# Kernel tuning notes

Measured on AMD Instinct MI355X. Metric: run time of the kernel, lower is better.

The kernel has to match this reference:

```python
import jax, jax.numpy as jnp
import numpy as np

B, S = 64, 256
VOCAB, DL, DA, DV = 30522, 300, 74, 35
DH, GH, LH, RH = 128, 64, 128, 128  # modality dim, proj-GRU hidden, LSTM hidden, RGN hidden


def _gru_dir(x, Wi, Wh, bi, bh):
    # x: [B,S,D] -> [B,S,H]; torch GRU gate order (r, z, n)
    xg = x @ Wi + bi  # [B,S,3H] precomputed input projections
    H = Wh.shape[0]
    def step(h, xg_t):
        hg = h @ Wh + bh
        xr, xz, xn = jnp.split(xg_t, 3, axis=-1)
        hr, hz, hn = jnp.split(hg, 3, axis=-1)
        r = jax.nn.sigmoid(xr + hr)
        z = jax.nn.sigmoid(xz + hz)
        n = jnp.tanh(xn + r * hn)
        h = (1.0 - z) * n + z * h
        return h, h
    h0 = jnp.zeros((x.shape[0], H), x.dtype)
    _, ys = jax.lax.scan(step, h0, jnp.swapaxes(xg, 0, 1))
    return jnp.swapaxes(ys, 0, 1)


def _bigru(x, Wi, Wh, bi, bh):
    f = _gru_dir(x, Wi[0], Wh[0], bi[0], bh[0])
    b = _gru_dir(x[:, ::-1], Wi[1], Wh[1], bi[1], bh[1])[:, ::-1]
    return jnp.concatenate([f, b], axis=-1)


def _lstm_dir(x, Wi, Wh, bi, bh):
    xg = x @ Wi + bi  # [B,S,4H]; torch LSTM gate order (i, f, g, o)
    H = Wh.shape[0]
    def step(carry, xg_t):
        h, c = carry
        g = xg_t + h @ Wh + bh
        i, f, gg, o = jnp.split(g, 4, axis=-1)
        c = jax.nn.sigmoid(f) * c + jax.nn.sigmoid(i) * jnp.tanh(gg)
        h = jax.nn.sigmoid(o) * jnp.tanh(c)
        return (h, c), h
    z = jnp.zeros((x.shape[0], H), x.dtype)
    _, ys = jax.lax.scan(step, (z, z), jnp.swapaxes(xg, 0, 1))
    return jnp.swapaxes(ys, 0, 1)


def _bilstm(x, Wi, Wh, bi, bh):
    f = _lstm_dir(x, Wi[0], Wh[0], bi[0], bh[0])
    b = _lstm_dir(x[:, ::-1], Wi[1], Wh[1], bi[1], bh[1])[:, ::-1]
    return jnp.concatenate([f, b], axis=-1)


def _rgn_scan(x, h0, Wx, Wh, b):
    # RGNCell: gated recurrent cell (GRU-style), returns final state [B,H]
    xg = x @ Wx + b  # [B,S,3H]
    def step(h, xg_t):
        hg = h @ Wh
        xr, xz, xn = jnp.split(xg_t, 3, axis=-1)
        hr, hz, hn = jnp.split(hg, 3, axis=-1)
        r = jax.nn.sigmoid(xr + hr)
        z = jax.nn.sigmoid(xz + hz)
        n = jnp.tanh(xn + r * hn)
        return (1.0 - z) * n + z * h, None
    h, _ = jax.lax.scan(step, h0, jnp.swapaxes(xg, 0, 1))
    return h


def _xattn(q, kv):
    # parameter-free scaled dot-product cross-modal attention (JCAF)
    scale = 1.0 / np.sqrt(q.shape[-1]).astype(np.float32)
    s = jnp.einsum('bsd,btd->bst', q, kv) * scale
    return jnp.einsum('bst,btd->bsd', jax.nn.softmax(s, axis=-1), kv)


def _forward(sentences, acoustic, video, state0, state1, emb,
             proj_l_W, proj_l_b, proj_a_W, proj_a_b, proj_v_W, proj_v_b,
             gru_Wi, gru_Wh, gru_bi, gru_bh,
             lstm_Wi, lstm_Wh, lstm_bi, lstm_bh,
             rgn_Wx, rgn_Wh, rgn_b, fc1_W, fc1_b, fc2_W, fc2_b):
    enc = emb[sentences]                          # LanguageEmbeddingLayer: [B,S,DL]
    # SeqEncoder: project each modality to 128-d (dropout off in eval)
    seq_l = enc @ proj_l_W + proj_l_b             # [B,S,128]
    seq_a = acoustic @ proj_a_W + proj_a_b
    seq_v = video @ proj_v_W + proj_v_b
    # project_l/a/v: bidirectional GRU 128 -> 2*64 = 128
    x_l = _bigru(seq_l, gru_Wi[0], gru_Wh[0], gru_bi[0], gru_bh[0])
    x_a = _bigru(seq_a, gru_Wi[1], gru_Wh[1], gru_bi[1], gru_bh[1])
    x_v = _bigru(seq_v, gru_Wi[2], gru_Wh[2], gru_bi[2], gru_bh[2])
    # JCAF: each modality enriched by cross-attention to the other two
    fin_txt = x_l + _xattn(x_l, x_a) + _xattn(x_l, x_v)
    fin_aud = x_a + _xattn(x_a, x_l) + _xattn(x_a, x_v)
    fin_vis = x_v + _xattn(x_v, x_l) + _xattn(x_v, x_a)
    tstep = jnp.concatenate([fin_txt, fin_aud, fin_vis], axis=-1)      # [B,S,384]
    step_fusion = _bilstm(tstep, lstm_Wi, lstm_Wh, lstm_bi, lstm_bh)   # [B,S,256]
    # two custom RGNCell recurrences: forward sweep + reversed sweep
    out0 = _rgn_scan(step_fusion, state0, rgn_Wx[0], rgn_Wh[0], rgn_b[0])
    out1 = _rgn_scan(step_fusion[:, ::-1], state1, rgn_Wx[1], rgn_Wh[1], rgn_b[1])
    h = jax.nn.leaky_relu((out0 + out1) @ fc1_W + fc1_b)
    return h @ fc2_W + fc2_b                     # [B,1]


def setup_inputs():
    keys = iter(jax.random.split(jax.random.key(0), 48))
    def rn(shape, s=0.05):
        return jax.random.normal(next(keys), shape, jnp.float32) * s
    return {
        'sentences': jax.random.randint(next(keys), (B, S), 0, VOCAB),
        'acoustic': jax.random.normal(next(keys), (B, S, DA), jnp.float32),
        'video': jax.random.normal(next(keys), (B, S, DV), jnp.float32),
        'state0': jax.random.normal(next(keys), (B, RH), jnp.float32),
        'state1': jax.random.normal(next(keys), (B, RH), jnp.float32),
        'emb': rn((VOCAB, DL), 0.1),
        'proj_l_W': rn((DL, DH)), 'proj_l_b': rn((DH,)),
        'proj_a_W': rn((DA, DH)), 'proj_a_b': rn((DH,)),
        'proj_v_W': rn((DV, DH)), 'proj_v_b': rn((DH,)),
        'gru_Wi': rn((3, 2, DH, 3 * GH)), 'gru_Wh': rn((3, 2, GH, 3 * GH)),
        'gru_bi': rn((3, 2, 3 * GH)), 'gru_bh': rn((3, 2, 3 * GH)),
        'lstm_Wi': rn((2, 3 * DH, 4 * LH)), 'lstm_Wh': rn((2, LH, 4 * LH)),
        'lstm_bi': rn((2, 4 * LH)), 'lstm_bh': rn((2, 4 * LH)),
        'rgn_Wx': rn((2, 2 * LH, 3 * RH)), 'rgn_Wh': rn((2, RH, 3 * RH)),
        'rgn_b': rn((2, 3 * RH)),
        'fc1_W': rn((RH, 32)), 'fc1_b': rn((32,)),
        'fc2_W': rn((32, 1)), 'fc2_b': rn((1,)),
    }


def reference(sentences, acoustic, video, state0, state1, emb,
              proj_l_W, proj_l_b, proj_a_W, proj_a_b, proj_v_W, proj_v_b,
              gru_Wi, gru_Wh, gru_bi, gru_bh,
              lstm_Wi, lstm_Wh, lstm_bi, lstm_bh,
              rgn_Wx, rgn_Wh, rgn_b, fc1_W, fc1_b, fc2_W, fc2_b):
    return _forward(sentences, acoustic, video, state0, state1, emb,
                    proj_l_W, proj_l_b, proj_a_W, proj_a_b, proj_v_W, proj_v_b,
                    gru_Wi, gru_Wh, gru_bi, gru_bh,
                    lstm_Wi, lstm_Wh, lstm_bi, lstm_bh,
                    rgn_Wx, rgn_Wh, rgn_b, fc1_W, fc1_b, fc2_W, fc2_b)
```

## Files before the change

kernel.cpp:

```cpp
#include <hip/hip_runtime.h>

#define WS_SEQ      0LL
#define WS_XGGRU    6291456LL
#define WS_X        0LL
#define WS_TSTEP    18874368LL
#define WS_S        6291456LL
#define WS_XGLSTM   0LL
#define WS_SF       16777216LL
#define WS_XGRGN    0LL
#define WS_OUT0     20971520LL

__device__ __forceinline__ float sigf(float x) { return 1.f / (1.f + __expf(-x)); }
__device__ __forceinline__ float rl(float v, int i) {
    return __int_as_float(__builtin_amdgcn_readlane(__float_as_int(v), i));
}

typedef float vf16 __attribute__((ext_vector_type(16)));

#define LD16(V, P, S) { _Pragma("unroll") \
    for (int _j = 0; _j < 16; ++_j) (V)[_j] = (P)[_j * (S)]; }
#define DOT16(ACC, V, H, B) { _Pragma("unroll") \
    for (int _j = 0; _j < 16; ++_j) (ACC) = fmaf(rl((H), (B) + _j), (V)[_j], (ACC)); }

__device__ __forceinline__ void gemm_body(
    const float* __restrict__ Ab, int lda, const int* __restrict__ idx,
    const float* __restrict__ Wb, int wld, int wtrans,
    const float* __restrict__ bb,
    float* __restrict__ Cb, int ldc,
    int K, float alpha, int accum)
{
    int m0 = blockIdx.y * 64, n0 = blockIdx.x * 64;
    int t = threadIdx.x;
    int tx = t & 7, ty = t >> 3;

    __shared__ __align__(16) float As[16][68];
    __shared__ __align__(16) float Ws[16][68];

    float acc[8][8];
#pragma unroll
    for (int i = 0; i < 8; ++i)
#pragma unroll
        for (int j = 0; j < 8; ++j) acc[i][j] = 0.f;

    long long arow[4];
#pragma unroll
    for (int i = 0; i < 4; ++i) {
        int m = (t + i * 64) >> 2;
        arow[i] = idx ? (long long)idx[m0 + m] : (long long)(m0 + m);
    }
    const bool a_vec = ((lda & 3) == 0);

    for (int k0 = 0; k0 < K; k0 += 16) {
#pragma unroll
        for (int i = 0; i < 4; ++i) {
            int j = t + i * 64;
            int m = j >> 2, kq = j & 3;
            int kk = k0 + kq * 4;
            const float* p = Ab + arow[i] * (long long)lda + kk;
            float4 v = {0.f, 0.f, 0.f, 0.f};
            if (a_vec && kk + 3 < K) {
                v = *(const float4*)p;
            } else {
                if (kk + 0 < K) v.x = p[0];
                if (kk + 1 < K) v.y = p[1];
                if (kk + 2 < K) v.z = p[2];
                if (kk + 3 < K) v.w = p[3];
            }
            As[kq * 4 + 0][m] = v.x; As[kq * 4 + 1][m] = v.y;
            As[kq * 4 + 2][m] = v.z; As[kq * 4 + 3][m] = v.w;
        }
        if (!wtrans) {
#pragma unroll
            for (int i = 0; i < 4; ++i) {
                int j = t + i * 64;
                int k = j >> 4, nq = j & 15;
                float4 v = {0.f, 0.f, 0.f, 0.f};
                if (k0 + k < K)
                    v = *(const float4*)(Wb + (long long)(k0 + k) * wld + n0 + nq * 4);
                *(float4*)&Ws[k][nq * 4] = v;
            }
        } else {
#pragma unroll
            for (int i = 0; i < 4; ++i) {
                int j = t + i * 64;
                int n = j >> 2, kq = j & 3;
                int kk = k0 + kq * 4;
                const float* p = Wb + (long long)(n0 + n) * wld + kk;
                float4 v = {0.f, 0.f, 0.f, 0.f};
                if (kk + 3 < K) v = *(const float4*)p;
                else {
                    if (kk + 0 < K) v.x = p[0];
                    if (kk + 1 < K) v.y = p[1];
                    if (kk + 2 < K) v.z = p[2];
                    if (kk + 3 < K) v.w = p[3];
                }
                Ws[kq * 4 + 0][n] = v.x; Ws[kq * 4 + 1][n] = v.y;
                Ws[kq * 4 + 2][n] = v.z; Ws[kq * 4 + 3][n] = v.w;
            }
        }
        __syncthreads();
#pragma unroll
        for (int k = 0; k < 16; ++k) {
            float4 a0 = *(const float4*)&As[k][ty * 8];
            float4 a1 = *(const float4*)&As[k][ty * 8 + 4];
            float4 b0 = *(const float4*)&Ws[k][tx * 8];
            float4 b1 = *(const float4*)&Ws[k][tx * 8 + 4];
            float av[8] = {a0.x, a0.y, a0.z, a0.w, a1.x, a1.y, a1.z, a1.w};
            float bv[8] = {b0.x, b0.y, b0.z, b0.w, b1.x, b1.y, b1.z, b1.w};
#pragma unroll
            for (int i = 0; i < 8; ++i)
#pragma unroll
                for (int j = 0; j < 8; ++j)
                    acc[i][j] = fmaf(av[i], bv[j], acc[i][j]);
        }
        __syncthreads();
    }

#pragma unroll
    for (int i = 0; i < 8; ++i) {
        long long gm = m0 + ty * 8 + i;
#pragma unroll
        for (int jq = 0; jq < 2; ++jq) {
            float* cp = Cb + gm * ldc + n0 + tx * 8 + jq * 4;
            float4 v;
            v.x = alpha * acc[i][jq * 4 + 0]; v.y = alpha * acc[i][jq * 4 + 1];
            v.z = alpha * acc[i][jq * 4 + 2]; v.w = alpha * acc[i][jq * 4 + 3];
            if (bb) {
                const float* bp = bb + n0 + tx * 8 + jq * 4;
                v.x += bp[0]; v.y += bp[1]; v.z += bp[2]; v.w += bp[3];
            }
            if (accum) {
                float4 o = *(const float4*)cp;
                v.x += o.x; v.y += o.y; v.z += o.z; v.w += o.w;
            }
            *(float4*)cp = v;
        }
    }
}

__global__ __launch_bounds__(64) void gemm_k(
    const float* __restrict__ A, long long a_z, int a_zdiv, int lda,
    const int* __restrict__ idx,
    const float* __restrict__ W, long long w_z, int wld, int wtrans,
    const float* __restrict__ bias, int bias_z,
    float* __restrict__ C, long long c_z, int ldc,
    int K, float alpha, int accum)
{
    int z = blockIdx.z;
    gemm_body(A + (long long)(z / a_zdiv) * a_z, lda, idx,
              W + (long long)z * w_z, wld, wtrans,
              bias ? bias + (long long)z * bias_z : nullptr,
              C + (long long)z * c_z, ldc, K, alpha, accum);
}

__global__ __launch_bounds__(64) void att_score_k(
    const float* __restrict__ X, float* __restrict__ S,
    int q0, int q1, int q2, int k0, int k1, int k2)
{
    int z = blockIdx.z;
    int pair = z >> 6, b = z & 63;
    int qi = pair == 0 ? q0 : (pair == 1 ? q1 : q2);
    int ki = pair == 0 ? k0 : (pair == 1 ? k1 : k2);
    gemm_body(X + (long long)qi * 2097152 + (long long)b * 32768, 128, nullptr,
              X + (long long)ki * 2097152 + (long long)b * 32768, 128, 1,
              nullptr,
              S + (long long)z * 65536, 256, 128, 0.08838834764831845f, 0);
}

__global__ __launch_bounds__(64) void att_apply_k(
    const float* __restrict__ S, const float* __restrict__ X,
    float* __restrict__ tstep,
    int q0, int q1, int q2, int k0, int k1, int k2)
{
    int z = blockIdx.z;
    int pair = z >> 6, b = z & 63;
    int qi = pair == 0 ? q0 : (pair == 1 ? q1 : q2);
    int ki = pair == 0 ? k0 : (pair == 1 ? k1 : k2);
    gemm_body(S + (long long)z * 65536, 256, nullptr,
              X + (long long)ki * 2097152 + (long long)b * 32768, 128, 0,
              nullptr,
              tstep + (long long)qi * 128 + (long long)b * 98304, 384,
              256, 1.f, 1);
}

__global__ __launch_bounds__(256) void copy_tstep_k(const float* __restrict__ x,
                                                    float* __restrict__ tstep)
{
    int o = blockIdx.x * 256 + threadIdx.x;
    int c = o % 384;
    int row = o / 384;
    int m = c >> 7, cc = c & 127;
    tstep[o] = x[(long long)m * 2097152 + (long long)row * 128 + cc];
}

__global__ __launch_bounds__(256) void softmax_k(float* __restrict__ S)
{
    int wave = threadIdx.x >> 6, lane = threadIdx.x & 63;
    int row = blockIdx.x * 4 + wave;
    float* p = S + (long long)row * 256;
    float v[4];
    float mx = -1e30f;
#pragma unroll
    for (int i = 0; i < 4; ++i) { v[i] = p[lane + i * 64]; mx = fmaxf(mx, v[i]); }
#pragma unroll
    for (int off = 32; off > 0; off >>= 1) mx = fmaxf(mx, __shfl_xor(mx, off));
    float sum = 0.f;
#pragma unroll
    for (int i = 0; i < 4; ++i) { v[i] = __expf(v[i] - mx); sum += v[i]; }
#pragma unroll
    for (int off = 32; off > 0; off >>= 1) sum += __shfl_xor(sum, off);
    float inv = 1.f / sum;
#pragma unroll
    for (int i = 0; i < 4; ++i) p[lane + i * 64] = v[i] * inv;
}

__global__ __launch_bounds__(192) void gru_rec_k(const float* __restrict__ xg,
                                                 const float* __restrict__ Wh,
                                                 const float* __restrict__ bh,
                                                 float* __restrict__ xout)
{
    int b = blockIdx.x, z = blockIdx.y;
    int m = z >> 1, d = z & 1;
    int tid = threadIdx.x, lane = tid & 63;
    int c = tid;
    const float* Whz = Wh + (long long)z * 12288;
    const float* wp = Whz + c;
    vf16 W0, W1, W2, W3;
    LD16(W0, wp + 0 * 16 * 192, 192); LD16(W1, wp + 1 * 16 * 192, 192);
    LD16(W2, wp + 2 * 16 * 192, 192); LD16(W3, wp + 3 * 16 * 192, 192);
    float bias = bh[z * 192 + c];

    __shared__ float hs[64];
    __shared__ float g[192];
    int n = tid;
    float h = 0.f;
    const float* xgb = xg + (long long)z * 3145728 + (long long)b * 49152;
    float* xob = xout + (long long)m * 2097152 + (long long)b * 32768 + d * 64;
    float x_r = 0, x_z = 0, x_n = 0;
    if (tid < 64) {
        hs[n] = 0.f;
        int tt0 = d ? 255 : 0;
        const float* xr = xgb + tt0 * 192;
        x_r = xr[n]; x_z = xr[64 + n]; x_n = xr[128 + n];
    }
    __syncthreads();

#pragma unroll 1
    for (int t = 0; t < 256; ++t) {
        int tt = d ? 255 - t : t;
        float nx_r = 0, nx_z = 0, nx_n = 0;
        if (tid < 64 && t < 255) {
            const float* xr = xgb + (d ? tt - 1 : tt + 1) * 192;
            nx_r = xr[n]; nx_z = xr[64 + n]; nx_n = xr[128 + n];
        }
        float hv = hs[lane];
        float s0 = bias, s1 = 0.f, s2 = 0.f, s3 = 0.f;
        DOT16(s0, W0, hv, 0);  DOT16(s1, W1, hv, 16);
        DOT16(s2, W2, hv, 32); DOT16(s3, W3, hv, 48);
        g[c] = (s0 + s1) + (s2 + s3);
        __syncthreads();
        if (tid < 64) {
            float r  = sigf(x_r + g[n]);
            float zz = sigf(x_z + g[64 + n]);
            float nn = tanhf(x_n + r * g[128 + n]);
            h = (1.f - zz) * nn + zz * h;
            hs[n] = h;
            xob[tt * 128 + n] = h;
            x_r = nx_r; x_z = nx_z; x_n = nx_n;
        }
        __syncthreads();
    }
}

__global__ __launch_bounds__(1024) void lstm_rec_k(const float* __restrict__ xg,
                                                   const float* __restrict__ Wh,
                                                   const float* __restrict__ bh,
                                                   float* __restrict__ sf)
{
    int b = blockIdx.x, d = blockIdx.y;
    int tid = threadIdx.x, lane = tid & 63;
    int kh = tid >> 9;
    int c  = tid & 511;
    const float* Whz = Wh + (long long)d * 65536;
    const float* wp = Whz + (long long)(kh * 64) * 512 + c;
    vf16 W0, W1, W2, W3;
    LD16(W0, wp + 0 * 16 * 512, 512); LD16(W1, wp + 1 * 16 * 512, 512);
    LD16(W2, wp + 2 * 16 * 512, 512); LD16(W3, wp + 3 * 16 * 512, 512);

    __shared__ float hs[128];
    __shared__ float part[1024];
    int n = tid;
    float b_i = 0, b_f = 0, b_g = 0, b_o = 0, h = 0.f, cst = 0.f;
    const float* xgb = xg + (long long)d * 8388608 + (long long)b * 131072;
    float* sfb = sf + (long long)b * 65536 + d * 128;
    float x_i = 0, x_f = 0, x_g = 0, x_o = 0;
    if (tid < 128) {
        b_i = bh[d * 512 + n];       b_f = bh[d * 512 + 128 + n];
        b_g = bh[d * 512 + 256 + n]; b_o = bh[d * 512 + 384 + n];
        hs[n] = 0.f;
        int tt0 = d ? 255 : 0;
        const float* xr = xgb + tt0 * 512;
        x_i = xr[n]; x_f = xr[128 + n]; x_g = xr[256 + n]; x_o = xr[384 + n];
    }
    __syncthreads();

#pragma unroll 1
    for (int t = 0; t < 256; ++t) {
        int tt = d ? 255 - t : t;
        float nx_i = 0, nx_f = 0, nx_g = 0, nx_o = 0;
        if (tid < 128 && t < 255) {
            const float* xr = xgb + (d ? tt - 1 : tt + 1) * 512;
            nx_i = xr[n]; nx_f = xr[128 + n]; nx_g = xr[256 + n]; nx_o = xr[384 + n];
        }
        float hv = hs[kh * 64 + lane];
        float s0 = 0.f, s1 = 0.f, s2 = 0.f, s3 = 0.f;
        DOT16(s0, W0, hv, 0);  DOT16(s1, W1, hv, 16);
        DOT16(s2, W2, hv, 32); DOT16(s3, W3, hv, 48);
        part[kh * 512 + c] = (s0 + s1) + (s2 + s3);
        __syncthreads();
        if (tid < 128) {
            float iv = part[n]       + part[512 + n]       + b_i + x_i;
            float fv = part[128 + n] + part[512 + 128 + n] + b_f + x_f;
            float gv = part[256 + n] + part[512 + 256 + n] + b_g + x_g;
            float ov = part[384 + n] + part[512 + 384 + n] + b_o + x_o;
            cst = sigf(fv) * cst + sigf(iv) * tanhf(gv);
            h = sigf(ov) * tanhf(cst);
            hs[n] = h;
            sfb[tt * 256 + n] = h;
            x_i = nx_i; x_f = nx_f; x_g = nx_g; x_o = nx_o;
        }
        __syncthreads();
    }
}

__global__ __launch_bounds__(768) void rgn_rec_k(const float* __restrict__ xg,
                                                 const float* __restrict__ Wh,
                                                 const float* __restrict__ state0,
                                                 const float* __restrict__ state1,
                                                 float* __restrict__ outbase)
{
    int b = blockIdx.x, d = blockIdx.y;
    int tid = threadIdx.x, lane = tid & 63;
    int kh = (tid >= 384) ? 1 : 0;
    int c  = tid - kh * 384;
    const float* Whz = Wh + (long long)d * 49152;
    const float* wp = Whz + (long long)(kh * 64) * 384 + c;
    vf16 W0, W1, W2, W3;
    LD16(W0, wp + 0 * 16 * 384, 384); LD16(W1, wp + 1 * 16 * 384, 384);
    LD16(W2, wp + 2 * 16 * 384, 384); LD16(W3, wp + 3 * 16 * 384, 384);

    __shared__ float hs[128];
    __shared__ float part[768];
    int n = tid;
    float h = 0.f;
    const float* st = d ? state1 : state0;
    const float* xgb = xg + (long long)d * 6291456 + (long long)b * 98304;
    float x_r = 0, x_z = 0, x_n = 0;
    if (tid < 128) {
        h = st[b * 128 + n];
        hs[n] = h;
        int tt0 = d ? 255 : 0;
        const float* xr = xgb + tt0 * 384;
        x_r = xr[n]; x_z = xr[128 + n]; x_n = xr[256 + n];
    }
    __syncthreads();

#pragma unroll 1
    for (int t = 0; t < 256; ++t) {
        int tt = d ? 255 - t : t;
        float nx_r = 0, nx_z = 0, nx_n = 0;
        if (tid < 128 && t < 255) {
            const float* xr = xgb + (d ? tt - 1 : tt + 1) * 384;
            nx_r = xr[n]; nx_z = xr[128 + n]; nx_n = xr[256 + n];
        }
        float hv = hs[kh * 64 + lane];
        float s0 = 0.f, s1 = 0.f, s2 = 0.f, s3 = 0.f;
        DOT16(s0, W0, hv, 0);  DOT16(s1, W1, hv, 16);
        DOT16(s2, W2, hv, 32); DOT16(s3, W3, hv, 48);
        part[kh * 384 + c] = (s0 + s1) + (s2 + s3);
        __syncthreads();
        if (tid < 128) {
            float pr = part[n]       + part[384 + n];
            float pz = part[128 + n] + part[384 + 128 + n];
            float pn = part[256 + n] + part[384 + 256 + n];
            float r  = sigf(x_r + pr);
            float zz = sigf(x_z + pz);
            float nn = tanhf(x_n + r * pn);
            h = (1.f - zz) * nn + zz * h;
            hs[n] = h;
            x_r = nx_r; x_z = nx_z; x_n = nx_n;
        }
        __syncthreads();
    }
    if (tid < 128) outbase[(long long)d * 8192 + b * 128 + n] = h;
}

__global__ __launch_bounds__(256) void fc_k(const float* __restrict__ o01,
                                            const float* __restrict__ f1W,
                                            const float* __restrict__ f1b,
                                            const float* __restrict__ f2W,
                                            const float* __restrict__ f2b,
                                            float* __restrict__ out)
{
    __shared__ float s[8192];
    __shared__ float h1[2048];
    int tid = threadIdx.x;
    for (int e = tid; e < 8192; e += 256) s[e] = o01[e] + o01[8192 + e];
    __syncthreads();
    for (int o = tid; o < 2048; o += 256) {
        int b = o >> 5, q = o & 31;
        float acc = f1b[q];
        for (int k = 0; k < 128; ++k) acc += s[b * 128 + k] * f1W[k * 32 + q];
        h1[o] = acc >= 0.f ? acc : 0.01f * acc;
    }
    __syncthreads();
    if (tid < 64) {
        float acc = f2b[0];
        for (int q = 0; q < 32; ++q) acc += h1[tid * 32 + q] * f2W[q];
        out[tid] = acc;
    }
}

extern "C" void kernel_launch(void* const* d_in, const int* in_sizes, int n_in,
                              void* d_out, int out_size, void* d_ws, size_t ws_size,
                              hipStream_t stream)
{
    const int*   sent     = (const int*)  d_in[0];
    const float* acoustic = (const float*)d_in[1];
    const float* video    = (const float*)d_in[2];
    const float* state0   = (const float*)d_in[3];
    const float* state1   = (const float*)d_in[4];
    const float* emb      = (const float*)d_in[5];
    const float* plW = (const float*)d_in[6],  *plb = (const float*)d_in[7];
    const float* paW = (const float*)d_in[8],  *pab = (const float*)d_in[9];
    const float* pvW = (const float*)d_in[10], *pvb = (const float*)d_in[11];
    const float* gWi = (const float*)d_in[12], *gWh = (const float*)d_in[13];
    const float* gbi = (const float*)d_in[14], *gbh = (const float*)d_in[15];
    const float* lWi = (const float*)d_in[16], *lWh = (const float*)d_in[17];
    const float* lbi = (const float*)d_in[18], *lbh = (const float*)d_in[19];
    const float* rWx = (const float*)d_in[20], *rWh = (const float*)d_in[21];
    const float* rb  = (const float*)d_in[22];
    const float* f1W = (const float*)d_in[23], *f1b = (const float*)d_in[24];
    const float* f2W = (const float*)d_in[25], *f2b = (const float*)d_in[26];
    float* ws  = (float*)d_ws;
    float* out = (float*)d_out;

    dim3 blk(64);

    gemm_k<<<dim3(2, 256, 1), blk, 0, stream>>>(emb, 0, 1, 300, sent,
        plW, 0, 128, 0, plb, 0, ws + WS_SEQ, 0, 128, 300, 1.f, 0);
    gemm_k<<<dim3(2, 256, 1), blk, 0, stream>>>(acoustic, 0, 1, 74, nullptr,
        paW, 0, 128, 0, pab, 0, ws + WS_SEQ + 2097152, 0, 128, 74, 1.f, 0);
    gemm_k<<<dim3(2, 256, 1), blk, 0, stream>>>(video, 0, 1, 35, nullptr,
        pvW, 0, 128, 0, pvb, 0, ws + WS_SEQ + 4194304, 0, 128, 35, 1.f, 0);

    gemm_k<<<dim3(3, 256, 6), blk, 0, stream>>>(ws + WS_SEQ, 2097152, 2, 128, nullptr,
        gWi, 24576, 192, 0, gbi, 192, ws + WS_XGGRU, 3145728, 192, 128, 1.f, 0);

    gru_rec_k<<<dim3(64, 6), dim3(192), 0, stream>>>(ws + WS_XGGRU, gWh, gbh, ws + WS_X);

    copy_tstep_k<<<dim3(24576), dim3(256), 0, stream>>>(ws + WS_X, ws + WS_TSTEP);

    att_score_k<<<dim3(4, 4, 192), blk, 0, stream>>>(ws + WS_X, ws + WS_S,
        0, 1, 2, 1, 0, 0);
    softmax_k<<<dim3(12288), dim3(256), 0, stream>>>(ws + WS_S);
    att_apply_k<<<dim3(2, 4, 192), blk, 0, stream>>>(ws + WS_S, ws + WS_X,
        ws + WS_TSTEP, 0, 1, 2, 1, 0, 0);
    att_score_k<<<dim3(4, 4, 192), blk, 0, stream>>>(ws + WS_X, ws + WS_S,
        0, 1, 2, 2, 2, 1);
    softmax_k<<<dim3(12288), dim3(256), 0, stream>>>(ws + WS_S);
    att_apply_k<<<dim3(2, 4, 192), blk, 0, stream>>>(ws + WS_S, ws + WS_X,
        ws + WS_TSTEP, 0, 1, 2, 2, 2, 1);

    gemm_k<<<dim3(8, 256, 2), blk, 0, stream>>>(ws + WS_TSTEP, 0, 1, 384, nullptr,
        lWi, 196608, 512, 0, lbi, 512, ws + WS_XGLSTM, 8388608, 512, 384, 1.f, 0);

    lstm_rec_k<<<dim3(64, 2), dim3(1024), 0, stream>>>(ws + WS_XGLSTM, lWh, lbh, ws + WS_SF);

    gemm_k<<<dim3(6, 256, 2), blk, 0, stream>>>(ws + WS_SF, 0, 1, 256, nullptr,
        rWx, 98304, 384, 0, rb, 384, ws + WS_XGRGN, 6291456, 384, 256, 1.f, 0);

    rgn_rec_k<<<dim3(64, 2), dim3(768), 0, stream>>>(ws + WS_XGRGN, rWh, state0, state1,
                                                     ws + WS_OUT0);

    fc_k<<<dim3(1), dim3(256), 0, stream>>>(ws + WS_OUT0, f1W, f1b, f2W, f2b, out);
}
```

Baseline: 1.697 ms.

## Compute gate updates redundantly per wave to drop LDS hidden-state exchange and second barrier

In the GRU, LSTM and RGN recurrent kernels, every wave now recomputes the gate nonlinearities for the hidden units it needs, keeping h in registers and broadcasting it by readlane. This removes the shared hs buffer and one __syncthreads per timestep, with the partial-sum buffer double-buffered so a single barrier suffices. The LSTM also folds input projection and bias into the dot-product accumulator. Sigmoid and tanh switch to rcp-based fast approximations, which trades some accuracy for shorter latency on the serial critical path.

```diff
diff --git a/kernel.cpp b/kernel.cpp
--- a/kernel.cpp
+++ b/kernel.cpp
@@ -10,7 +10,13 @@
 #define WS_XGRGN    0LL
 #define WS_OUT0     20971520LL
 
-__device__ __forceinline__ float sigf(float x) { return 1.f / (1.f + __expf(-x)); }
+__device__ __forceinline__ float sigf(float x) {
+    return __builtin_amdgcn_rcpf(1.f + __expf(-x));
+}
+__device__ __forceinline__ float tanhfast(float x) {
+    float e = __expf(2.f * x);
+    return 1.f - 2.f * __builtin_amdgcn_rcpf(e + 1.f);
+}
 __device__ __forceinline__ float rl(float v, int i) {
     return __int_as_float(__builtin_amdgcn_readlane(__float_as_int(v), i));
 }
@@ -230,45 +236,35 @@
     LD16(W2, wp + 2 * 16 * 192, 192); LD16(W3, wp + 3 * 16 * 192, 192);
     float bias = bh[z * 192 + c];
 
-    __shared__ float hs[64];
-    __shared__ float g[192];
-    int n = tid;
+    __shared__ float g[2][192];
+    int n = lane;
     float h = 0.f;
     const float* xgb = xg + (long long)z * 3145728 + (long long)b * 49152;
     float* xob = xout + (long long)m * 2097152 + (long long)b * 32768 + d * 64;
-    float x_r = 0, x_z = 0, x_n = 0;
-    if (tid < 64) {
-        hs[n] = 0.f;
-        int tt0 = d ? 255 : 0;
-        const float* xr = xgb + tt0 * 192;
-        x_r = xr[n]; x_z = xr[64 + n]; x_n = xr[128 + n];
-    }
-    __syncthreads();
+    int tt0 = d ? 255 : 0;
+    const float* xr0 = xgb + tt0 * 192;
+    float x_r = xr0[n], x_z = xr0[64 + n], x_n = xr0[128 + n];
 
 #pragma unroll 1
     for (int t = 0; t < 256; ++t) {
         int tt = d ? 255 - t : t;
         float nx_r = 0, nx_z = 0, nx_n = 0;
-        if (tid < 64 && t < 255) {
+        if (t < 255) {
             const float* xr = xgb + (d ? tt - 1 : tt + 1) * 192;
             nx_r = xr[n]; nx_z = xr[64 + n]; nx_n = xr[128 + n];
         }
-        float hv = hs[lane];
         float s0 = bias, s1 = 0.f, s2 = 0.f, s3 = 0.f;
-        DOT16(s0, W0, hv, 0);  DOT16(s1, W1, hv, 16);
-        DOT16(s2, W2, hv, 32); DOT16(s3, W3, hv, 48);
-        g[c] = (s0 + s1) + (s2 + s3);
+        DOT16(s0, W0, h, 0);  DOT16(s1, W1, h, 16);
+        DOT16(s2, W2, h, 32); DOT16(s3, W3, h, 48);
+        g[t & 1][c] = (s0 + s1) + (s2 + s3);
         __syncthreads();
-        if (tid < 64) {
-            float r  = sigf(x_r + g[n]);
-            float zz = sigf(x_z + g[64 + n]);
-            float nn = tanhf(x_n + r * g[128 + n]);
-            h = (1.f - zz) * nn + zz * h;
-            hs[n] = h;
-            xob[tt * 128 + n] = h;
-            x_r = nx_r; x_z = nx_z; x_n = nx_n;
-        }
-        __syncthreads();
+        const float* gp = g[t & 1];
+        float r  = sigf(x_r + gp[n]);
+        float zz = sigf(x_z + gp[64 + n]);
+        float nn = tanhfast(x_n + r * gp[128 + n]);
+        h = (1.f - zz) * nn + zz * h;
+        if (c < 64) xob[tt * 128 + n] = h;
+        x_r = nx_r; x_z = nx_z; x_n = nx_n;
     }
 }
 
@@ -287,49 +283,39 @@
     LD16(W0, wp + 0 * 16 * 512, 512); LD16(W1, wp + 1 * 16 * 512, 512);
     LD16(W2, wp + 2 * 16 * 512, 512); LD16(W3, wp + 3 * 16 * 512, 512);
 
-    __shared__ float hs[128];
-    __shared__ float part[1024];
-    int n = tid;
-    float b_i = 0, b_f = 0, b_g = 0, b_o = 0, h = 0.f, cst = 0.f;
+    __shared__ float part[2][1024];
+    int n = kh * 64 + lane;
+    float h = 0.f, cst = 0.f;
     const float* xgb = xg + (long long)d * 8388608 + (long long)b * 131072;
     float* sfb = sf + (long long)b * 65536 + d * 128;
-    float x_i = 0, x_f = 0, x_g = 0, x_o = 0;
-    if (tid < 128) {
-        b_i = bh[d * 512 + n];       b_f = bh[d * 512 + 128 + n];
-        b_g = bh[d * 512 + 256 + n]; b_o = bh[d * 512 + 384 + n];
-        hs[n] = 0.f;
+
+    float bias = 0.f, xc = 0.f;
+    if (kh == 0) {
+        bias = bh[d * 512 + c];
         int tt0 = d ? 255 : 0;
-        const float* xr = xgb + tt0 * 512;
-        x_i = xr[n]; x_f = xr[128 + n]; x_g = xr[256 + n]; x_o = xr[384 + n];
-    }
-    __syncthreads();
+        xc = xgb[tt0 * 512 + c];
+    }
 
 #pragma unroll 1
     for (int t = 0; t < 256; ++t) {
         int tt = d ? 255 - t : t;
-        float nx_i = 0, nx_f = 0, nx_g = 0, nx_o = 0;
-        if (tid < 128 && t < 255) {
-            const float* xr = xgb + (d ? tt - 1 : tt + 1) * 512;
-            nx_i = xr[n]; nx_f = xr[128 + n]; nx_g = xr[256 + n]; nx_o = xr[384 + n];
-        }
-        float hv = hs[kh * 64 + lane];
-        float s0 = 0.f, s1 = 0.f, s2 = 0.f, s3 = 0.f;
-        DOT16(s0, W0, hv, 0);  DOT16(s1, W1, hv, 16);
-        DOT16(s2, W2, hv, 32); DOT16(s3, W3, hv, 48);
-        part[kh * 512 + c] = (s0 + s1) + (s2 + s3);
+        float nxc = 0.f;
+        if (kh == 0 && t < 255)
+            nxc = xgb[(d ? tt - 1 : tt + 1) * 512 + c];
+        float s0 = xc + bias, s1 = 0.f, s2 = 0.f, s3 = 0.f;
+        DOT16(s0, W0, h, 0);  DOT16(s1, W1, h, 16);
+        DOT16(s2, W2, h, 32); DOT16(s3, W3, h, 48);
+        part[t & 1][kh * 512 + c] = (s0 + s1) + (s2 + s3);
         __syncthreads();
-        if (tid < 128) {
-            float iv = part[n]       + part[512 + n]       + b_i + x_i;
-            float fv = part[128 + n] + part[512 + 128 + n] + b_f + x_f;
-            float gv = part[256 + n] + part[512 + 256 + n] + b_g + x_g;
-            float ov = part[384 + n] + part[512 + 384 + n] + b_o + x_o;
-            cst = sigf(fv) * cst + sigf(iv) * tanhf(gv);
-            h = sigf(ov) * tanhf(cst);
-            hs[n] = h;
-            sfb[tt * 256 + n] = h;
-            x_i = nx_i; x_f = nx_f; x_g = nx_g; x_o = nx_o;
-        }
-        __syncthreads();
+        const float* p = part[t & 1];
+        float iv = p[n]       + p[512 + n];
+        float fv = p[128 + n] + p[512 + 128 + n];
+        float gv = p[256 + n] + p[512 + 256 + n];
+        float ov = p[384 + n] + p[512 + 384 + n];
+        cst = sigf(fv) * cst + sigf(iv) * tanhfast(gv);
+        h = sigf(ov) * tanhfast(cst);
+        if (c < 64) sfb[tt * 256 + n] = h;
+        xc = nxc;
     }
 }
 
@@ -349,50 +335,39 @@
     LD16(W0, wp + 0 * 16 * 384, 384); LD16(W1, wp + 1 * 16 * 384, 384);
     LD16(W2, wp + 2 * 16 * 384, 384); LD16(W3, wp + 3 * 16 * 384, 384);
 
-    __shared__ float hs[128];
-    __shared__ float part[768];
-    int n = tid;
-    float h = 0.f;
+    __shared__ float part[2][768];
+    int n = kh * 64 + lane;
     const float* st = d ? state1 : state0;
+    float h = st[b * 128 + n];
     const float* xgb = xg + (long long)d * 6291456 + (long long)b * 98304;
-    float x_r = 0, x_z = 0, x_n = 0;
-    if (tid < 128) {
-        h = st[b * 128 + n];
-        hs[n] = h;
-        int tt0 = d ? 255 : 0;
-        const float* xr = xgb + tt0 * 384;
-        x_r = xr[n]; x_z = xr[128 + n]; x_n = xr[256 + n];
-    }
-    __syncthreads();
+    int tt0 = d ? 255 : 0;
+    const float* xr0 = xgb + tt0 * 384;
+    float x_r = xr0[n], x_z = xr0[128 + n], x_n = xr0[256 + n];
 
 #pragma unroll 1
     for (int t = 0; t < 256; ++t) {
         int tt = d ? 255 - t : t;
         float nx_r = 0, nx_z = 0, nx_n = 0;
-        if (tid < 128 && t < 255) {
+        if (t < 255) {
             const float* xr = xgb + (d ? tt - 1 : tt + 1) * 384;
             nx_r = xr[n]; nx_z = xr[128 + n]; nx_n = xr[256 + n];
         }
-        float hv = hs[kh * 64 + lane];
         float s0 = 0.f, s1 = 0.f, s2 = 0.f, s3 = 0.f;
-        DOT16(s0, W0, hv, 0);  DOT16(s1, W1, hv, 16);
-        DOT16(s2, W2, hv, 32); DOT16(s3, W3, hv, 48);
-        part[kh * 384 + c] = (s0 + s1) + (s2 + s3);
+        DOT16(s0, W0, h, 0);  DOT16(s1, W1, h, 16);
+        DOT16(s2, W2, h, 32); DOT16(s3, W3, h, 48);
+        part[t & 1][kh * 384 + c] = (s0 + s1) + (s2 + s3);
         __syncthreads();
-        if (tid < 128) {
-            float pr = part[n]       + part[384 + n];
-            float pz = part[128 + n] + part[384 + 128 + n];
-            float pn = part[256 + n] + part[384 + 256 + n];
-            float r  = sigf(x_r + pr);
-            float zz = sigf(x_z + pz);
-            float nn = tanhf(x_n + r * pn);
-            h = (1.f - zz) * nn + zz * h;
-            hs[n] = h;
-            x_r = nx_r; x_z = nx_z; x_n = nx_n;
-        }
-        __syncthreads();
-    }
-    if (tid < 128) outbase[(long long)d * 8192 + b * 128 + n] = h;
+        const float* p = part[t & 1];
+        float pr = p[n]       + p[384 + n];
+        float pz = p[128 + n] + p[384 + 128 + n];
+        float pn = p[256 + n] + p[384 + 256 + n];
+        float r  = sigf(x_r + pr);
+        float zz = sigf(x_z + pz);
+        float nn = tanhfast(x_n + r * pn);
+        h = (1.f - zz) * nn + zz * h;
+        x_r = nx_r; x_z = nx_z; x_n = nx_n;
+    }
+    if (c < 64) outbase[(long long)d * 8192 + b * 128 + n] = h;
 }
 
 __global__ __launch_bounds__(256) void fc_k(const float* __restrict__ o01,
```

After: 1.654 ms. 2.6% less time.
